# Kernel tuning notes

Measured on AMD Instinct MI355X. Metric: run time of the kernel, lower is better.

## Reference

```python
import jax, jax.numpy as jnp
import numpy as np

B, T, CIN, H = 128, 512, 512, 256  # batch, time, conv-in channels, hidden
G = 4 * H  # LSTM gate width (i,f,g,o in PyTorch order)


def setup_inputs() -> dict:
    key = jax.random.key(0)
    ks = jax.random.split(key, 13)
    s = 0.05
    return {
        "x": jax.random.normal(ks[0], (B, CIN, T, 1), jnp.float32),
        "w1": jax.random.normal(ks[1], (H, CIN), jnp.float32) * s,  # 1x1 conv -> [out,in]
        "b1": jax.random.normal(ks[2], (H,), jnp.float32) * s,
        "w2": jax.random.normal(ks[3], (H, H), jnp.float32) * s,
        "b2": jax.random.normal(ks[4], (H,), jnp.float32) * s,
        "w_ih_f": jax.random.normal(ks[5], (G, H), jnp.float32) * s,
        "w_hh_f": jax.random.normal(ks[6], (G, H), jnp.float32) * s,
        "b_ih_f": jax.random.normal(ks[7], (G,), jnp.float32) * s,
        "b_hh_f": jax.random.normal(ks[8], (G,), jnp.float32) * s,
        "w_ih_b": jax.random.normal(ks[9], (G, H), jnp.float32) * s,
        "w_hh_b": jax.random.normal(ks[10], (G, H), jnp.float32) * s,
        "b_ih_b": jax.random.normal(ks[11], (G,), jnp.float32) * s,
        "b_hh_b": jax.random.normal(ks[12], (G,), jnp.float32) * s,
    }


def _lstm(xg, w_hh):
    """Run LSTM over time. xg: [B,T,4H] = x@w_ih.T + b_ih + b_hh (precomputed)."""
    h0 = jnp.zeros((xg.shape[0], w_hh.shape[1]), xg.dtype)

    def step(carry, g_in):
        h, c = carry
        g = g_in + h @ w_hh.T
        i, f, gg, o = jnp.split(g, 4, axis=-1)
        c = jax.nn.sigmoid(f) * c + jax.nn.sigmoid(i) * jnp.tanh(gg)
        h = jax.nn.sigmoid(o) * jnp.tanh(c)
        return (h, c), h

    _, hs = jax.lax.scan(step, (h0, h0), jnp.swapaxes(xg, 0, 1))  # [T,B,H]
    return jnp.swapaxes(hs, 0, 1)  # [B,T,H]


def reference(x, w1, b1, w2, b2, w_ih_f, w_hh_f, b_ih_f, b_hh_f,
              w_ih_b, w_hh_b, b_ih_b, b_hh_b):
    # 1x1 convs == per-pixel GEMMs
    y = jax.nn.relu(jnp.einsum('bchw,oc->bohw', x, w1) + b1[None, :, None, None])
    y = jax.nn.relu(jnp.einsum('bchw,oc->bohw', y, w2) + b2[None, :, None, None])
    # torch .view(B, H_dim, -1) on contiguous [B,256,T,1] -> [B,T,256] (row-major reinterpret)
    seq = y.reshape(y.shape[0], y.shape[2], -1)  # [B,T,256]
    # forward direction
    xg_f = jnp.einsum('btd,gd->btg', seq, w_ih_f) + b_ih_f + b_hh_f
    h_f = _lstm(xg_f, w_hh_f)
    # backward direction: reverse time, run, reverse back
    seq_r = seq[:, ::-1, :]
    xg_b = jnp.einsum('btd,gd->btg', seq_r, w_ih_b) + b_ih_b + b_hh_b
    h_b = _lstm(xg_b, w_hh_b)[:, ::-1, :]
    out = jnp.concatenate([h_f, h_b], axis=-1)  # [B,T,2H]
    # dropout is identity at inference; return last timestep
    return out[:, -1, :]
```

## Files before the change

### kernel.cpp

```cpp
#include <hip/hip_runtime.h>
#include <math.h>

#define BATCH 128
#define TT 512
#define CIN 512
#define HID 256
#define GG 1024

typedef _Float16 half2_t __attribute__((ext_vector_type(2)));
typedef _Float16 half8_t __attribute__((ext_vector_type(8)));
typedef float f32x4_t __attribute__((ext_vector_type(4)));

__device__ __forceinline__ float sigf(float x) { return 1.f / (1.f + __expf(-x)); }
__device__ __forceinline__ float tanhf_(float x) {
    float a = fabsf(x);
    float e = __expf(-2.f * a);
    float r = (1.f - e) / (1.f + e);
    return copysignf(r, x);
}
__device__ __forceinline__ float fdot2_(half2_t a, half2_t b, float c) {
#if __has_builtin(__builtin_amdgcn_fdot2)
    return __builtin_amdgcn_fdot2(a, b, c, false);
#else
    return c + (float)a.x * (float)b.x + (float)a.y * (float)b.y;
#endif
}

__global__ void prep_cast(const float* __restrict__ w1, const float* __restrict__ w2,
                          const float* __restrict__ wih, const float* __restrict__ bih,
                          const float* __restrict__ bhh,
                          _Float16* __restrict__ w1h, _Float16* __restrict__ w2h,
                          _Float16* __restrict__ wihh, float* __restrict__ bsum)
{
    const int i = blockIdx.x * 256 + threadIdx.x;
    if (i < 131072) w1h[i] = (_Float16)w1[i];
    if (i < 65536)  w2h[i] = (_Float16)w2[i];
    if (i < 262144) wihh[i] = (_Float16)wih[i];
    if (i < 1024)   bsum[i] = bih[i] + bhh[i];
}

__global__ __launch_bounds__(256) void cast_transpose_x(
    const float* __restrict__ x, _Float16* __restrict__ xt)
{
    const int b = blockIdx.z, c0 = blockIdx.y * 64, t0 = blockIdx.x * 64;
    __shared__ float tl[64][68];
    const float* xb = x + (size_t)b * CIN * TT;
    const int tid = threadIdx.x;
    const int lt = (tid & 15) * 4, lc = tid >> 4;
    #pragma unroll
    for (int r = 0; r < 4; ++r) {
        const int c = lc + r * 16;
        float4 v = *(const float4*)(xb + (size_t)(c0 + c) * TT + t0 + lt);
        tl[c][lt] = v.x; tl[c][lt + 1] = v.y; tl[c][lt + 2] = v.z; tl[c][lt + 3] = v.w;
    }
    __syncthreads();
    const int trow = tid >> 2, coff = (tid & 3) * 16;
    _Float16 o[16];
    #pragma unroll
    for (int i = 0; i < 16; ++i) o[i] = (_Float16)tl[coff + i][trow];
    _Float16* dst = xt + (size_t)b * TT * CIN + (size_t)(t0 + trow) * CIN + c0 + coff;
    *(float4*)dst = *(float4*)&o[0];
    *(float4*)(dst + 8) = *(float4*)&o[8];
}

template <int RELU, int BIASROW>
__global__ __launch_bounds__(256, 4) void mfma_nt(
    const _Float16* __restrict__ A, const _Float16* __restrict__ B,
    const float* __restrict__ bias, _Float16* __restrict__ C,
    int M, int N, int K, long sA, long sB, long sC)
{
    __shared__ __align__(16) char smem[34816];
    _Float16 (*As)[40] = (_Float16(*)[40])smem;
    _Float16 (*Bs)[40] = (_Float16(*)[40])(smem + 10240);
    float (*Ct)[132] = (float(*)[132])smem;

    const int nb = blockIdx.z;
    A += (size_t)nb * sA; B += (size_t)nb * sB; C += (size_t)nb * sC;
    const int m0 = blockIdx.y * 128, n0 = blockIdx.x * 128;
    const int tid = threadIdx.x;
    const int wave = tid >> 6, lane = tid & 63;
    const int quad = lane >> 4, l15 = lane & 15;
    const int wm = (wave >> 1) * 64, wn = (wave & 1) * 64;
    const int srow = tid >> 1, sko = (tid & 1) * 16;

    f32x4_t acc[4][4];
    const f32x4_t zz = {0.f, 0.f, 0.f, 0.f};
    #pragma unroll
    for (int i = 0; i < 4; ++i)
        #pragma unroll
        for (int j = 0; j < 4; ++j) acc[i][j] = zz;

    for (int k0 = 0; k0 < K; k0 += 32) {
        {
            const float4* ga = (const float4*)(A + (size_t)(m0 + srow) * K + k0 + sko);
            float4 a0 = ga[0], a1 = ga[1];
            const float4* gb = (const float4*)(B + (size_t)(n0 + srow) * K + k0 + sko);
            float4 b0 = gb[0], b1 = gb[1];
            *(float4*)&As[srow][sko] = a0; *(float4*)&As[srow][sko + 8] = a1;
            *(float4*)&Bs[srow][sko] = b0; *(float4*)&Bs[srow][sko + 8] = b1;
        }
        __syncthreads();
        half8_t af[4], bf[4];
        #pragma unroll
        for (int i = 0; i < 4; ++i) af[i] = *(const half8_t*)&As[wm + i * 16 + l15][quad * 8];
        #pragma unroll
        for (int j = 0; j < 4; ++j) bf[j] = *(const half8_t*)&Bs[wn + j * 16 + l15][quad * 8];
        #pragma unroll
        for (int i = 0; i < 4; ++i)
            #pragma unroll
            for (int j = 0; j < 4; ++j)
                acc[i][j] = __builtin_amdgcn_mfma_f32_16x16x32_f16(af[i], bf[j], acc[i][j], 0, 0, 0);
        __syncthreads();
    }

    const int trow = tid >> 2, coff = (tid & 3) * 32;
    float bcol[32];
    if (!BIASROW) {
        #pragma unroll
        for (int i = 0; i < 8; ++i)
            *(float4*)&bcol[i * 4] = *(const float4*)&bias[n0 + coff + i * 4];
    }
    #pragma unroll
    for (int p = 0; p < 2; ++p) {
        if (p) __syncthreads();
        if ((wave >> 1) == p) {
            #pragma unroll
            for (int mi = 0; mi < 4; ++mi)
                #pragma unroll
                for (int ni = 0; ni < 4; ++ni)
                    #pragma unroll
                    for (int r = 0; r < 4; ++r)
                        Ct[mi * 16 + quad * 4 + r][wn + ni * 16 + l15] = acc[mi][ni][r];
        }
        __syncthreads();
        float brow = 0.f;
        if (BIASROW) brow = bias[m0 + p * 64 + trow];
        float vv[32];
        #pragma unroll
        for (int i = 0; i < 8; ++i) *(float4*)&vv[i * 4] = *(float4*)&Ct[trow][coff + i * 4];
        _Float16 o[32];
        #pragma unroll
        for (int i = 0; i < 32; ++i) {
            float v = vv[i] + (BIASROW ? brow : bcol[i]);
            if (RELU) v = fmaxf(v, 0.f);
            o[i] = (_Float16)v;
        }
        _Float16* dst = C + (size_t)(m0 + p * 64 + trow) * N + n0 + coff;
        #pragma unroll
        for (int i = 0; i < 4; ++i) *(float4*)(dst + i * 8) = *(float4*)&o[i * 8];
    }
}

__global__ __launch_bounds__(1024, 4) void lstm_scan5(
    const _Float16* __restrict__ xg, const float* __restrict__ whh,
    float* __restrict__ out, unsigned long long* __restrict__ xb)
{
    const int tid = threadIdx.x;
    const int bid = blockIdx.x;
    const int is_hi = (bid >= 128) ? 1 : 0;
    const int g = is_hi ? bid - 128 : bid;
    const int q4 = tid >> 8;
    const int s = tid & 255;
    const int u = s & 127;
    const int rowA = (s >> 7) * 256 + is_hi * 128 + u;
    const int rowB = rowA + 512;

    __shared__ __align__(16) unsigned int hsh[128];
    __shared__ float psh[2048];

    half2_t wA[32], wB[32];
    {
        const float4* pa = (const float4*)(whh + (size_t)rowA * 256 + q4 * 64);
        const float4* pb = (const float4*)(whh + (size_t)rowB * 256 + q4 * 64);
        #pragma unroll
        for (int k = 0; k < 16; ++k) {
            float4 a = pa[k], b = pb[k];
            wA[2 * k + 0] = half2_t{(_Float16)a.x, (_Float16)a.y};
            wA[2 * k + 1] = half2_t{(_Float16)a.z, (_Float16)a.w};
            wB[2 * k + 0] = half2_t{(_Float16)b.x, (_Float16)b.y};
            wB[2 * k + 1] = half2_t{(_Float16)b.z, (_Float16)b.w};
        }
    }
    if (tid < 128) hsh[tid] = 0u;
    const _Float16* xgb = xg + (size_t)g * TT * GG;
    float xA = 0.f, xB = 0.f;
    if (q4 == 0) { xA = (float)xgb[rowA]; xB = (float)xgb[rowB]; }
    float c0 = 0.f, c1 = 0.f, hk0 = 0.f, hk1 = 0.f;
    __syncthreads();

    for (int t = 0; t < TT; ++t) {
        const float vA = xA, vB = xB;
        if (q4 == 0 && t < TT - 1) {
            xA = (float)xgb[(size_t)(t + 1) * GG + rowA];
            xB = (float)xgb[(size_t)(t + 1) * GG + rowB];
        }
        float aA0 = 0.f, aA1 = 0.f, aB0 = 0.f, aB1 = 0.f;
        const float4* hp = (const float4*)hsh + q4 * 8;
        #pragma unroll
        for (int kk = 0; kk < 8; ++kk) {
            const float4 hv = hp[kk];
            const half2_t h0 = __builtin_bit_cast(half2_t, hv.x);
            const half2_t h1 = __builtin_bit_cast(half2_t, hv.y);
            const half2_t h2 = __builtin_bit_cast(half2_t, hv.z);
            const half2_t h3 = __builtin_bit_cast(half2_t, hv.w);
            aA0 = fdot2_(wA[4 * kk + 0], h0, aA0);
            aA1 = fdot2_(wA[4 * kk + 1], h1, aA1);
            aA0 = fdot2_(wA[4 * kk + 2], h2, aA0);
            aA1 = fdot2_(wA[4 * kk + 3], h3, aA1);
            aB0 = fdot2_(wB[4 * kk + 0], h0, aB0);
            aB1 = fdot2_(wB[4 * kk + 1], h1, aB1);
            aB0 = fdot2_(wB[4 * kk + 2], h2, aB0);
            aB1 = fdot2_(wB[4 * kk + 3], h3, aB1);
        }
        psh[q4 * 512 + s]       = aA0 + aA1 + vA;
        psh[q4 * 512 + 256 + s] = aB0 + aB1 + vB;
        __syncthreads();
        if (tid < 64) {
            const int l = tid;
            float2 gate[4];
            #pragma unroll
            for (int gg = 0; gg < 4; ++gg) {
                float2 sum = {0.f, 0.f};
                #pragma unroll
                for (int qq = 0; qq < 4; ++qq) {
                    const float2 v = *(const float2*)&psh[qq * 512 + gg * 128 + 2 * l];
                    sum.x += v.x; sum.y += v.y;
                }
                gate[gg] = sum;
            }
            const float i0 = sigf(gate[0].x), i1 = sigf(gate[0].y);
            const float f0 = sigf(gate[1].x), f1 = sigf(gate[1].y);
            const float g0 = tanhf_(gate[2].x), g1 = tanhf_(gate[2].y);
            const float o0 = sigf(gate[3].x), o1 = sigf(gate[3].y);
            c0 = f0 * c0 + i0 * g0;  hk0 = o0 * tanhf_(c0);
            c1 = f1 * c1 + i1 * g1;  hk1 = o1 * tanhf_(c1);
            const unsigned int u0 =
                (unsigned int)__builtin_bit_cast(unsigned short, (_Float16)hk0);
            const unsigned int u1 =
                (unsigned int)__builtin_bit_cast(unsigned short, (_Float16)hk1);
            hsh[is_hi * 64 + l] = u0 | (u1 << 16);
            if (t < TT - 1) {
                const unsigned int tg = (unsigned int)(t + 1) << 16;
                const unsigned long long pk =
                    ((unsigned long long)(tg | u1) << 32) | (unsigned long long)(tg | u0);
                __hip_atomic_store(&xb[((size_t)g * 2 + is_hi) * 64 + l], pk,
                                   __ATOMIC_RELAXED, __HIP_MEMORY_SCOPE_AGENT);
                asm volatile("" ::: "memory");
                unsigned long long v;
                const unsigned long long* src = &xb[((size_t)g * 2 + (1 - is_hi)) * 64 + l];
                for (;;) {
                    v = __hip_atomic_load(src, __ATOMIC_RELAXED,
                                          __HIP_MEMORY_SCOPE_AGENT);
                    if ((((v >> 16) & 0xFFFFu) == (unsigned)(t + 1)) &&
                        ((unsigned)(v >> 48) == (unsigned)(t + 1))) break;
                    __builtin_amdgcn_s_sleep(1);
                }
                hsh[(1 - is_hi) * 64 + l] =
                    (unsigned int)(v & 0xFFFFu) |
                    ((unsigned int)((v >> 32) & 0xFFFFu) << 16);
            }
        }
        __syncthreads();
    }
    if (tid < 64) {
        out[(size_t)g * 512 + is_hi * 128 + 2 * tid + 0] = hk0;
        out[(size_t)g * 512 + is_hi * 128 + 2 * tid + 1] = hk1;
    }
}

__global__ __launch_bounds__(256) void lstm_back_last(
    const _Float16* __restrict__ y2h, const float* __restrict__ wih,
    const float* __restrict__ bih, const float* __restrict__ bhh,
    float* __restrict__ out)
{
    const int b = blockIdx.x;
    const int t = threadIdx.x;
    __shared__ float s[256];
    s[t] = (float)y2h[(size_t)b * (HID * TT) + (TT - 1) * HID + t];
    __syncthreads();
    float acc[4];
    #pragma unroll
    for (int q = 0; q < 4; ++q) acc[q] = bih[t + q * 256] + bhh[t + q * 256];
    #pragma unroll
    for (int q = 0; q < 4; ++q) {
        const float* w = wih + (size_t)(t + q * 256) * 256;
        float a = acc[q];
        for (int k = 0; k < 256; k += 4) {
            const float4 w4 = *(const float4*)&w[k];
            const float4 h4 = *(const float4*)&s[k];
            a += w4.x * h4.x; a += w4.y * h4.y;
            a += w4.z * h4.z; a += w4.w * h4.w;
        }
        acc[q] = a;
    }
    const float i = sigf(acc[0]);
    const float g = tanhf_(acc[2]), o = sigf(acc[3]);
    const float c = i * g;
    const float h = o * tanhf_(c);
    out[(size_t)b * 512 + 256 + t] = h;
}

extern "C" void kernel_launch(void* const* d_in, const int* in_sizes, int n_in,
                              void* d_out, int out_size, void* d_ws, size_t ws_size,
                              hipStream_t stream) {
    const float* x      = (const float*)d_in[0];
    const float* w1     = (const float*)d_in[1];
    const float* b1     = (const float*)d_in[2];
    const float* w2     = (const float*)d_in[3];
    const float* b2     = (const float*)d_in[4];
    const float* w_ih_f = (const float*)d_in[5];
    const float* w_hh_f = (const float*)d_in[6];
    const float* b_ih_f = (const float*)d_in[7];
    const float* b_hh_f = (const float*)d_in[8];
    const float* w_ih_b = (const float*)d_in[9];
    const float* b_ih_b = (const float*)d_in[11];
    const float* b_hh_b = (const float*)d_in[12];
    float* out = (float*)d_out;

    char* ws = (char*)d_ws;
    _Float16* xgh  = (_Float16*)(ws);
    _Float16* xt   = (_Float16*)(ws + 134217728);
    _Float16* y1t  = (_Float16*)(ws + 201326592);
    _Float16* y2h  = (_Float16*)(ws + 234881024);
    _Float16* w1h  = (_Float16*)(ws + 268435456);
    _Float16* w2h  = (_Float16*)(ws + 268697600);
    _Float16* wihh = (_Float16*)(ws + 268828672);
    float*    bsum = (float*)   (ws + 269352960);
    unsigned long long* xb = (unsigned long long*)(ws + 269357056);

    prep_cast<<<1024, 256, 0, stream>>>(w1, w2, w_ih_f, b_ih_f, b_hh_f,
                                        w1h, w2h, wihh, bsum);
    cast_transpose_x<<<dim3(8, 8, BATCH), 256, 0, stream>>>(x, xt);
    mfma_nt<1, 0><<<dim3(2, 4, BATCH), 256, 0, stream>>>(
        xt, w1h, b1, y1t, 512, 256, 512, 512L * 512, 0, 512L * 256);
    mfma_nt<1, 1><<<dim3(4, 2, BATCH), 256, 0, stream>>>(
        w2h, y1t, b2, y2h, 256, 512, 256, 0, 512L * 256, 256L * 512);
    mfma_nt<0, 0><<<dim3(8, 512, 1), 256, 0, stream>>>(
        y2h, wihh, bsum, xgh, 65536, 1024, 256, 0, 0, 0);
    lstm_back_last<<<BATCH, 256, 0, stream>>>(y2h, w_ih_b, b_ih_b, b_hh_b, out);
    lstm_scan5<<<256, 1024, 0, stream>>>(xgh, w_hh_f, out, xb);
}
```

Before: 1.282 ms.

## Interleave two batch rows per LSTM block to overlap dot products with cross-block handoff

Each scan block now handles two batch rows, processed in an interleaved schedule. While one wave does the activation and publishes h for batch A, the other waves compute the recurrent dot products for batch B, and a dedicated wave polls the partner block's h. This hides the inter-block exchange latency and the serial activation phase behind useful work. The cost is half as many blocks, more syncthreads per step and double the shared buffers.

```diff
diff --git a/kernel.cpp b/kernel.cpp
--- a/kernel.cpp
+++ b/kernel.cpp
@@ -151,22 +151,24 @@
     }
 }
 
-__global__ __launch_bounds__(1024, 4) void lstm_scan5(
+__global__ __launch_bounds__(1024, 4) void lstm_scan6(
     const _Float16* __restrict__ xg, const float* __restrict__ whh,
     float* __restrict__ out, unsigned long long* __restrict__ xb)
 {
     const int tid = threadIdx.x;
     const int bid = blockIdx.x;
-    const int is_hi = (bid >= 128) ? 1 : 0;
-    const int g = is_hi ? bid - 128 : bid;
+    const int is_hi = (bid >= 64) ? 1 : 0;
+    const int p = is_hi ? bid - 64 : bid;
+    const int gb0 = 2 * p, gb1 = 2 * p + 1;
     const int q4 = tid >> 8;
     const int s = tid & 255;
     const int u = s & 127;
     const int rowA = (s >> 7) * 256 + is_hi * 128 + u;
     const int rowB = rowA + 512;
-
-    __shared__ __align__(16) unsigned int hsh[128];
-    __shared__ float psh[2048];
+    const int wv = tid >> 6, l = tid & 63;
+
+    __shared__ __align__(16) unsigned int hsh[2][128];
+    __shared__ __align__(16) float psh[2][2048];
 
     half2_t wA[32], wB[32];
     {
@@ -181,21 +183,21 @@
             wB[2 * k + 1] = half2_t{(_Float16)b.z, (_Float16)b.w};
         }
     }
-    if (tid < 128) hsh[tid] = 0u;
-    const _Float16* xgb = xg + (size_t)g * TT * GG;
-    float xA = 0.f, xB = 0.f;
-    if (q4 == 0) { xA = (float)xgb[rowA]; xB = (float)xgb[rowB]; }
+    if (tid < 256) hsh[tid >> 7][tid & 127] = 0u;
+
+    const _Float16* xgb0 = xg + (size_t)gb0 * TT * GG;
+    const _Float16* xgb1 = xg + (size_t)gb1 * TT * GG;
+    float x0A = 0.f, x0B = 0.f, x1A = 0.f, x1B = 0.f;
+    if (q4 == 1) {
+        x0A = (float)xgb0[rowA]; x0B = (float)xgb0[rowB];
+        x1A = (float)xgb1[rowA]; x1B = (float)xgb1[rowB];
+    }
     float c0 = 0.f, c1 = 0.f, hk0 = 0.f, hk1 = 0.f;
     __syncthreads();
 
-    for (int t = 0; t < TT; ++t) {
-        const float vA = xA, vB = xB;
-        if (q4 == 0 && t < TT - 1) {
-            xA = (float)xgb[(size_t)(t + 1) * GG + rowA];
-            xB = (float)xgb[(size_t)(t + 1) * GG + rowB];
-        }
+    auto dot_phase = [&](int bb, float vA, float vB) {
         float aA0 = 0.f, aA1 = 0.f, aB0 = 0.f, aB1 = 0.f;
-        const float4* hp = (const float4*)hsh + q4 * 8;
+        const float4* hp = (const float4*)&hsh[bb][0] + q4 * 8;
         #pragma unroll
         for (int kk = 0; kk < 8; ++kk) {
             const float4 hv = hp[kk];
@@ -212,59 +214,82 @@
             aB0 = fdot2_(wB[4 * kk + 2], h2, aB0);
             aB1 = fdot2_(wB[4 * kk + 3], h3, aB1);
         }
-        psh[q4 * 512 + s]       = aA0 + aA1 + vA;
-        psh[q4 * 512 + 256 + s] = aB0 + aB1 + vB;
-        __syncthreads();
-        if (tid < 64) {
-            const int l = tid;
-            float2 gate[4];
+        psh[bb][q4 * 512 + s]       = aA0 + aA1 + vA;
+        psh[bb][q4 * 512 + 256 + s] = aB0 + aB1 + vB;
+    };
+
+    auto act_publish = [&](int bb, int gbb, int t) {
+        float2 gate[4];
+        #pragma unroll
+        for (int gg = 0; gg < 4; ++gg) {
+            float2 sum = {0.f, 0.f};
             #pragma unroll
-            for (int gg = 0; gg < 4; ++gg) {
-                float2 sum = {0.f, 0.f};
-                #pragma unroll
-                for (int qq = 0; qq < 4; ++qq) {
-                    const float2 v = *(const float2*)&psh[qq * 512 + gg * 128 + 2 * l];
-                    sum.x += v.x; sum.y += v.y;
-                }
-                gate[gg] = sum;
+            for (int qq = 0; qq < 4; ++qq) {
+                const float2 v = *(const float2*)&psh[bb][qq * 512 + gg * 128 + 2 * l];
+                sum.x += v.x; sum.y += v.y;
             }
-            const float i0 = sigf(gate[0].x), i1 = sigf(gate[0].y);
-            const float f0 = sigf(gate[1].x), f1 = sigf(gate[1].y);
-            const float g0 = tanhf_(gate[2].x), g1 = tanhf_(gate[2].y);
-            const float o0 = sigf(gate[3].x), o1 = sigf(gate[3].y);
-            c0 = f0 * c0 + i0 * g0;  hk0 = o0 * tanhf_(c0);
-            c1 = f1 * c1 + i1 * g1;  hk1 = o1 * tanhf_(c1);
-            const unsigned int u0 =
-                (unsigned int)__builtin_bit_cast(unsigned short, (_Float16)hk0);
-            const unsigned int u1 =
-                (unsigned int)__builtin_bit_cast(unsigned short, (_Float16)hk1);
-            hsh[is_hi * 64 + l] = u0 | (u1 << 16);
-            if (t < TT - 1) {
-                const unsigned int tg = (unsigned int)(t + 1) << 16;
-                const unsigned long long pk =
-                    ((unsigned long long)(tg | u1) << 32) | (unsigned long long)(tg | u0);
-                __hip_atomic_store(&xb[((size_t)g * 2 + is_hi) * 64 + l], pk,
-                                   __ATOMIC_RELAXED, __HIP_MEMORY_SCOPE_AGENT);
-                asm volatile("" ::: "memory");
-                unsigned long long v;
-                const unsigned long long* src = &xb[((size_t)g * 2 + (1 - is_hi)) * 64 + l];
-                for (;;) {
-                    v = __hip_atomic_load(src, __ATOMIC_RELAXED,
-                                          __HIP_MEMORY_SCOPE_AGENT);
-                    if ((((v >> 16) & 0xFFFFu) == (unsigned)(t + 1)) &&
-                        ((unsigned)(v >> 48) == (unsigned)(t + 1))) break;
-                    __builtin_amdgcn_s_sleep(1);
-                }
-                hsh[(1 - is_hi) * 64 + l] =
-                    (unsigned int)(v & 0xFFFFu) |
-                    ((unsigned int)((v >> 32) & 0xFFFFu) << 16);
-            }
-        }
-        __syncthreads();
-    }
-    if (tid < 64) {
-        out[(size_t)g * 512 + is_hi * 128 + 2 * tid + 0] = hk0;
-        out[(size_t)g * 512 + is_hi * 128 + 2 * tid + 1] = hk1;
+            gate[gg] = sum;
+        }
+        const float i0 = sigf(gate[0].x), i1 = sigf(gate[0].y);
+        const float f0 = sigf(gate[1].x), f1 = sigf(gate[1].y);
+        const float q0 = tanhf_(gate[2].x), q1 = tanhf_(gate[2].y);
+        const float o0 = sigf(gate[3].x), o1 = sigf(gate[3].y);
+        c0 = f0 * c0 + i0 * q0;  hk0 = o0 * tanhf_(c0);
+        c1 = f1 * c1 + i1 * q1;  hk1 = o1 * tanhf_(c1);
+        const unsigned int u0 =
+            (unsigned int)__builtin_bit_cast(unsigned short, (_Float16)hk0);
+        const unsigned int u1 =
+            (unsigned int)__builtin_bit_cast(unsigned short, (_Float16)hk1);
+        if (t < TT - 1) {
+            const unsigned int tg = (unsigned int)(t + 1) << 16;
+            const unsigned long long pk =
+                ((unsigned long long)(tg | u1) << 32) | (unsigned long long)(tg | u0);
+            __hip_atomic_store(&xb[((size_t)gbb * 2 + is_hi) * 64 + l], pk,
+                               __ATOMIC_RELAXED, __HIP_MEMORY_SCOPE_AGENT);
+            asm volatile("" ::: "memory");
+        }
+        hsh[bb][is_hi * 64 + l] = u0 | (u1 << 16);
+    };
+
+    auto poll_partner = [&](int bb, int gbb, unsigned int tag) {
+        const unsigned long long* src = &xb[((size_t)gbb * 2 + (1 - is_hi)) * 64 + l];
+        unsigned long long v;
+        for (;;) {
+            v = __hip_atomic_load(src, __ATOMIC_RELAXED, __HIP_MEMORY_SCOPE_AGENT);
+            if ((((v >> 16) & 0xFFFFu) == tag) && ((unsigned)(v >> 48) == tag)) break;
+            __builtin_amdgcn_s_sleep(1);
+        }
+        hsh[bb][(1 - is_hi) * 64 + l] =
+            (unsigned int)(v & 0xFFFFu) | ((unsigned int)((v >> 32) & 0xFFFFu) << 16);
+    };
+
+    for (int t = 0; t < TT; ++t) {
+        const float v0A = x0A, v0B = x0B, v1A = x1A, v1B = x1B;
+        if (q4 == 1 && t < TT - 1) {
+            x0A = (float)xgb0[(size_t)(t + 1) * GG + rowA];
+            x0B = (float)xgb0[(size_t)(t + 1) * GG + rowB];
+            x1A = (float)xgb1[(size_t)(t + 1) * GG + rowA];
+            x1B = (float)xgb1[(size_t)(t + 1) * GG + rowB];
+        }
+        if (wv == 15 && t > 0) poll_partner(1, gb1, (unsigned int)t);
+        dot_phase(0, v0A, v0B);
+        __syncthreads();
+
+        if (wv == 0) act_publish(0, gb0, t);
+        dot_phase(1, v1A, v1B);
+        __syncthreads();
+
+        if (wv == 1) act_publish(1, gb1, t);
+        if (wv == 15 && t < TT - 1) poll_partner(0, gb0, (unsigned int)(t + 1));
+        __syncthreads();
+    }
+    if (wv == 0) {
+        out[(size_t)gb0 * 512 + is_hi * 128 + 2 * l + 0] = hk0;
+        out[(size_t)gb0 * 512 + is_hi * 128 + 2 * l + 1] = hk1;
+    }
+    if (wv == 1) {
+        out[(size_t)gb1 * 512 + is_hi * 128 + 2 * l + 0] = hk0;
+        out[(size_t)gb1 * 512 + is_hi * 128 + 2 * l + 1] = hk1;
     }
 }
 
@@ -338,5 +363,5 @@
     mfma_nt<0, 0><<<dim3(8, 512, 1), 256, 0, stream>>>(
         y2h, wihh, bsum, xgh, 65536, 1024, 256, 0, 0, 0);
     lstm_back_last<<<BATCH, 256, 0, stream>>>(y2h, w_ih_b, b_ih_b, b_hh_b, out);
-    lstm_scan5<<<256, 1024, 0, stream>>>(xgh, w_hh_f, out, xb);
-}
+    lstm_scan6<<<128, 1024, 0, stream>>>(xgh, w_hh_f, out, xb);
+}
```

After: 1.630 ms. +27.2%, slower.

## Run each batch's LSTM scan in one workgroup, dropping cross-block handshakes

Applied to the files above, without the earlier changes.

Replaces the two-workgroups-per-batch-row LSTM scan, which swapped hidden-state halves through global atomics and spin-waits every step, with one 1024-thread workgroup per batch row. Each thread now computes all four gates for one hidden unit. Three gate weight slices sit in registers and the output-gate weights go in a swizzled 128KB LDS buffer. The gate pre-activations are staged in a double-buffered LDS slot. This removes per-step inter-block sync latency, but halves the number of workgroups (128 instead of 256) and adds more per-thread work plus LDS weight reads each step.

```diff
diff --git a/kernel.cpp b/kernel.cpp
--- a/kernel.cpp
+++ b/kernel.cpp
@@ -151,51 +151,73 @@
     }
 }
 
-__global__ __launch_bounds__(1024, 4) void lstm_scan5(
+__global__ __launch_bounds__(1024, 4) void lstm_scan7(
     const _Float16* __restrict__ xg, const float* __restrict__ whh,
-    float* __restrict__ out, unsigned long long* __restrict__ xb)
-{
+    float* __restrict__ out)
+{
+    __shared__ __align__(16) _Float16 wlds[256 * 256];
+    __shared__ __align__(16) float psh[4096];
+    __shared__ __align__(16) _Float16 xgsh[2][1024];
+    __shared__ __align__(16) _Float16 hshh[256];
+
     const int tid = threadIdx.x;
-    const int bid = blockIdx.x;
-    const int is_hi = (bid >= 128) ? 1 : 0;
-    const int g = is_hi ? bid - 128 : bid;
-    const int q4 = tid >> 8;
-    const int s = tid & 255;
-    const int u = s & 127;
-    const int rowA = (s >> 7) * 256 + is_hi * 128 + u;
-    const int rowB = rowA + 512;
-
-    __shared__ __align__(16) unsigned int hsh[128];
-    __shared__ float psh[2048];
-
-    half2_t wA[32], wB[32];
+    const int b   = blockIdx.x;
+    const int q4  = tid >> 8;
+    const int s   = tid & 255;
+    const _Float16* xgb = xg + (size_t)b * TT * GG;
+
     {
-        const float4* pa = (const float4*)(whh + (size_t)rowA * 256 + q4 * 64);
-        const float4* pb = (const float4*)(whh + (size_t)rowB * 256 + q4 * 64);
+        const int sr = tid >> 2, c4 = tid & 3;
+        const float* wr = whh + (size_t)(768 + sr) * 256;
+        #pragma unroll
+        for (int j = 0; j < 8; ++j) {
+            const int g = c4 * 8 + j;
+            const float4 w0 = *(const float4*)&wr[g * 8 + 0];
+            const float4 w1 = *(const float4*)&wr[g * 8 + 4];
+            float4 pk;
+            half2_t* pp = (half2_t*)&pk;
+            pp[0] = half2_t{(_Float16)w0.x, (_Float16)w0.y};
+            pp[1] = half2_t{(_Float16)w0.z, (_Float16)w0.w};
+            pp[2] = half2_t{(_Float16)w1.x, (_Float16)w1.y};
+            pp[3] = half2_t{(_Float16)w1.z, (_Float16)w1.w};
+            *(float4*)((char*)wlds + sr * 512 + ((g ^ (sr & 7)) << 4)) = pk;
+        }
+    }
+    half2_t wI[32], wF[32], wGt[32];
+    {
+        const float4* pi = (const float4*)(whh + (size_t)(s)*256 + q4 * 64);
+        const float4* pf = (const float4*)(whh + (size_t)(s + 256) * 256 + q4 * 64);
+        const float4* pg = (const float4*)(whh + (size_t)(s + 512) * 256 + q4 * 64);
         #pragma unroll
         for (int k = 0; k < 16; ++k) {
-            float4 a = pa[k], b = pb[k];
-            wA[2 * k + 0] = half2_t{(_Float16)a.x, (_Float16)a.y};
-            wA[2 * k + 1] = half2_t{(_Float16)a.z, (_Float16)a.w};
-            wB[2 * k + 0] = half2_t{(_Float16)b.x, (_Float16)b.y};
-            wB[2 * k + 1] = half2_t{(_Float16)b.z, (_Float16)b.w};
-        }
-    }
-    if (tid < 128) hsh[tid] = 0u;
-    const _Float16* xgb = xg + (size_t)g * TT * GG;
-    float xA = 0.f, xB = 0.f;
-    if (q4 == 0) { xA = (float)xgb[rowA]; xB = (float)xgb[rowB]; }
-    float c0 = 0.f, c1 = 0.f, hk0 = 0.f, hk1 = 0.f;
+            const float4 a = pi[k];
+            wI[2 * k + 0] = half2_t{(_Float16)a.x, (_Float16)a.y};
+            wI[2 * k + 1] = half2_t{(_Float16)a.z, (_Float16)a.w};
+            const float4 f = pf[k];
+            wF[2 * k + 0] = half2_t{(_Float16)f.x, (_Float16)f.y};
+            wF[2 * k + 1] = half2_t{(_Float16)f.z, (_Float16)f.w};
+            const float4 g = pg[k];
+            wGt[2 * k + 0] = half2_t{(_Float16)g.x, (_Float16)g.y};
+            wGt[2 * k + 1] = half2_t{(_Float16)g.z, (_Float16)g.w};
+        }
+    }
+    if (tid < 128) ((unsigned int*)hshh)[tid] = 0u;
+    if (q4 == 3) {
+        *(uint2*)&xgsh[0][4 * s] = *(const uint2*)&xgb[4 * s];
+    }
+    float c = 0.f, hlast = 0.f;
     __syncthreads();
 
+    const float4* hp = (const float4*)hshh + q4 * 8;
+    const char* wob = (const char*)wlds + s * 512 + q4 * 128;
+    const int sw3 = s & 7;
+
     for (int t = 0; t < TT; ++t) {
-        const float vA = xA, vB = xB;
-        if (q4 == 0 && t < TT - 1) {
-            xA = (float)xgb[(size_t)(t + 1) * GG + rowA];
-            xB = (float)xgb[(size_t)(t + 1) * GG + rowB];
-        }
-        float aA0 = 0.f, aA1 = 0.f, aB0 = 0.f, aB1 = 0.f;
-        const float4* hp = (const float4*)hsh + q4 * 8;
+        if (q4 == 3 && t + 1 < TT) {
+            *(uint2*)&xgsh[(t + 1) & 1][4 * s] =
+                *(const uint2*)&xgb[(size_t)(t + 1) * GG + 4 * s];
+        }
+        float aI = 0.f, aF = 0.f, aG = 0.f, aO = 0.f;
         #pragma unroll
         for (int kk = 0; kk < 8; ++kk) {
             const float4 hv = hp[kk];
@@ -203,69 +225,51 @@
             const half2_t h1 = __builtin_bit_cast(half2_t, hv.y);
             const half2_t h2 = __builtin_bit_cast(half2_t, hv.z);
             const half2_t h3 = __builtin_bit_cast(half2_t, hv.w);
-            aA0 = fdot2_(wA[4 * kk + 0], h0, aA0);
-            aA1 = fdot2_(wA[4 * kk + 1], h1, aA1);
-            aA0 = fdot2_(wA[4 * kk + 2], h2, aA0);
-            aA1 = fdot2_(wA[4 * kk + 3], h3, aA1);
-            aB0 = fdot2_(wB[4 * kk + 0], h0, aB0);
-            aB1 = fdot2_(wB[4 * kk + 1], h1, aB1);
-            aB0 = fdot2_(wB[4 * kk + 2], h2, aB0);
-            aB1 = fdot2_(wB[4 * kk + 3], h3, aB1);
-        }
-        psh[q4 * 512 + s]       = aA0 + aA1 + vA;
-        psh[q4 * 512 + 256 + s] = aB0 + aB1 + vB;
-        __syncthreads();
-        if (tid < 64) {
-            const int l = tid;
-            float2 gate[4];
-            #pragma unroll
-            for (int gg = 0; gg < 4; ++gg) {
-                float2 sum = {0.f, 0.f};
-                #pragma unroll
-                for (int qq = 0; qq < 4; ++qq) {
-                    const float2 v = *(const float2*)&psh[qq * 512 + gg * 128 + 2 * l];
-                    sum.x += v.x; sum.y += v.y;
-                }
-                gate[gg] = sum;
-            }
-            const float i0 = sigf(gate[0].x), i1 = sigf(gate[0].y);
-            const float f0 = sigf(gate[1].x), f1 = sigf(gate[1].y);
-            const float g0 = tanhf_(gate[2].x), g1 = tanhf_(gate[2].y);
-            const float o0 = sigf(gate[3].x), o1 = sigf(gate[3].y);
-            c0 = f0 * c0 + i0 * g0;  hk0 = o0 * tanhf_(c0);
-            c1 = f1 * c1 + i1 * g1;  hk1 = o1 * tanhf_(c1);
-            const unsigned int u0 =
-                (unsigned int)__builtin_bit_cast(unsigned short, (_Float16)hk0);
-            const unsigned int u1 =
-                (unsigned int)__builtin_bit_cast(unsigned short, (_Float16)hk1);
-            hsh[is_hi * 64 + l] = u0 | (u1 << 16);
-            if (t < TT - 1) {
-                const unsigned int tg = (unsigned int)(t + 1) << 16;
-                const unsigned long long pk =
-                    ((unsigned long long)(tg | u1) << 32) | (unsigned long long)(tg | u0);
-                __hip_atomic_store(&xb[((size_t)g * 2 + is_hi) * 64 + l], pk,
-                                   __ATOMIC_RELAXED, __HIP_MEMORY_SCOPE_AGENT);
-                asm volatile("" ::: "memory");
-                unsigned long long v;
-                const unsigned long long* src = &xb[((size_t)g * 2 + (1 - is_hi)) * 64 + l];
-                for (;;) {
-                    v = __hip_atomic_load(src, __ATOMIC_RELAXED,
-                                          __HIP_MEMORY_SCOPE_AGENT);
-                    if ((((v >> 16) & 0xFFFFu) == (unsigned)(t + 1)) &&
-                        ((unsigned)(v >> 48) == (unsigned)(t + 1))) break;
-                    __builtin_amdgcn_s_sleep(1);
-                }
-                hsh[(1 - is_hi) * 64 + l] =
-                    (unsigned int)(v & 0xFFFFu) |
-                    ((unsigned int)((v >> 32) & 0xFFFFu) << 16);
-            }
-        }
-        __syncthreads();
-    }
-    if (tid < 64) {
-        out[(size_t)g * 512 + is_hi * 128 + 2 * tid + 0] = hk0;
-        out[(size_t)g * 512 + is_hi * 128 + 2 * tid + 1] = hk1;
-    }
+            const float4 wv = *(const float4*)(wob + ((kk ^ sw3) << 4));
+            const half2_t o0 = __builtin_bit_cast(half2_t, wv.x);
+            const half2_t o1 = __builtin_bit_cast(half2_t, wv.y);
+            const half2_t o2 = __builtin_bit_cast(half2_t, wv.z);
+            const half2_t o3 = __builtin_bit_cast(half2_t, wv.w);
+            aI = fdot2_(wI[4 * kk + 0], h0, aI);
+            aI = fdot2_(wI[4 * kk + 1], h1, aI);
+            aI = fdot2_(wI[4 * kk + 2], h2, aI);
+            aI = fdot2_(wI[4 * kk + 3], h3, aI);
+            aF = fdot2_(wF[4 * kk + 0], h0, aF);
+            aF = fdot2_(wF[4 * kk + 1], h1, aF);
+            aF = fdot2_(wF[4 * kk + 2], h2, aF);
+            aF = fdot2_(wF[4 * kk + 3], h3, aF);
+            aG = fdot2_(wGt[4 * kk + 0], h0, aG);
+            aG = fdot2_(wGt[4 * kk + 1], h1, aG);
+            aG = fdot2_(wGt[4 * kk + 2], h2, aG);
+            aG = fdot2_(wGt[4 * kk + 3], h3, aG);
+            aO = fdot2_(o0, h0, aO);
+            aO = fdot2_(o1, h1, aO);
+            aO = fdot2_(o2, h2, aO);
+            aO = fdot2_(o3, h3, aO);
+        }
+        psh[q4 * 1024 + s]       = aI;
+        psh[q4 * 1024 + s + 256] = aF;
+        psh[q4 * 1024 + s + 512] = aG;
+        psh[q4 * 1024 + s + 768] = aO;
+        __syncthreads();
+        if (tid < 256) {
+            const int cur = t & 1;
+            const float gi = psh[s] + psh[1024 + s] + psh[2048 + s] + psh[3072 + s]
+                             + (float)xgsh[cur][s];
+            const float gf = psh[s + 256] + psh[1280 + s] + psh[2304 + s] + psh[3328 + s]
+                             + (float)xgsh[cur][s + 256];
+            const float gq = psh[s + 512] + psh[1536 + s] + psh[2560 + s] + psh[3584 + s]
+                             + (float)xgsh[cur][s + 512];
+            const float go = psh[s + 768] + psh[1792 + s] + psh[2816 + s] + psh[3840 + s]
+                             + (float)xgsh[cur][s + 768];
+            const float iv = sigf(gi), fv = sigf(gf), gv = tanhf_(gq), ov = sigf(go);
+            c = fv * c + iv * gv;
+            hlast = ov * tanhf_(c);
+            hshh[s] = (_Float16)hlast;
+        }
+        __syncthreads();
+    }
+    if (tid < 256) out[(size_t)b * 512 + s] = hlast;
 }
 
 __global__ __launch_bounds__(256) void lstm_back_last(
@@ -326,7 +330,6 @@
     _Float16* w2h  = (_Float16*)(ws + 268697600);
     _Float16* wihh = (_Float16*)(ws + 268828672);
     float*    bsum = (float*)   (ws + 269352960);
-    unsigned long long* xb = (unsigned long long*)(ws + 269357056);
 
     prep_cast<<<1024, 256, 0, stream>>>(w1, w2, w_ih_f, b_ih_f, b_hh_f,
                                         w1h, w2h, wihh, bsum);
@@ -338,5 +341,5 @@
     mfma_nt<0, 0><<<dim3(8, 512, 1), 256, 0, stream>>>(
         y2h, wihh, bsum, xgh, 65536, 1024, 256, 0, 0, 0);
     lstm_back_last<<<BATCH, 256, 0, stream>>>(y2h, w_ih_b, b_ih_b, b_hh_b, out);
-    lstm_scan5<<<256, 1024, 0, stream>>>(xgh, w_hh_f, out, xb);
-}
+    lstm_scan7<<<BATCH, 1024, 0, stream>>>(xgh, w_hh_f, out);
+}
```

Result: slower. 1.422 ms (+11.0%).

## Pipeline cross-block spin-wait loads and double-buffer mailbox by step parity

Applied to the files above, without the earlier changes.

Reworks the inter-block hidden-state exchange in the LSTM scan. The mailbox is now double-buffered by timestep parity and zeroed in lstm_back_last. It reuses the y1t workspace region, which is dead by the time the scan runs. The poll is an inline-assembly loop that keeps three pairs of global loads in flight instead of a serialized load-sleep loop, with a fallback to the old atomic poll after a bounded number of tries. The aim is lower per-step handshake latency on the serial critical path. The cost is fragile hand-written asm, and the parity buffers rely on the peer never running more than one step ahead.

```diff
diff --git a/kernel.cpp b/kernel.cpp
--- a/kernel.cpp
+++ b/kernel.cpp
@@ -151,9 +151,9 @@
     }
 }
 
-__global__ __launch_bounds__(1024, 4) void lstm_scan5(
+__global__ __launch_bounds__(1024, 4) void lstm_scan11(
     const _Float16* __restrict__ xg, const float* __restrict__ whh,
-    float* __restrict__ out, unsigned long long* __restrict__ xb)
+    float* __restrict__ out, unsigned long long* __restrict__ mb)
 {
     const int tid = threadIdx.x;
     const int bid = blockIdx.x;
@@ -238,26 +238,105 @@
                 (unsigned int)__builtin_bit_cast(unsigned short, (_Float16)hk0);
             const unsigned int u1 =
                 (unsigned int)__builtin_bit_cast(unsigned short, (_Float16)hk1);
-            hsh[is_hi * 64 + l] = u0 | (u1 << 16);
             if (t < TT - 1) {
-                const unsigned int tg = (unsigned int)(t + 1) << 16;
+                const unsigned int want = (unsigned int)(t + 1);
+                const unsigned int tg = want << 16;
                 const unsigned long long pk =
                     ((unsigned long long)(tg | u1) << 32) | (unsigned long long)(tg | u0);
-                __hip_atomic_store(&xb[((size_t)g * 2 + is_hi) * 64 + l], pk,
+                const size_t par = (size_t)(want & 1u) * 16384;
+                __hip_atomic_store(&mb[par + ((size_t)g * 2 + is_hi) * 64 + l], pk,
                                    __ATOMIC_RELAXED, __HIP_MEMORY_SCOPE_AGENT);
                 asm volatile("" ::: "memory");
-                unsigned long long v;
-                const unsigned long long* src = &xb[((size_t)g * 2 + (1 - is_hi)) * 64 + l];
-                for (;;) {
-                    v = __hip_atomic_load(src, __ATOMIC_RELAXED,
-                                          __HIP_MEMORY_SCOPE_AGENT);
-                    if ((((v >> 16) & 0xFFFFu) == (unsigned)(t + 1)) &&
-                        ((unsigned)(v >> 48) == (unsigned)(t + 1))) break;
-                    __builtin_amdgcn_s_sleep(1);
+                hsh[is_hi * 64 + l] = u0 | (u1 << 16);
+                const unsigned long long srcaddr = (unsigned long long)
+                    &mb[par + ((size_t)g * 2 + (1 - is_hi)) * 64 + l];
+                unsigned int r0, r1, hit;
+                {
+                    unsigned int pa0, pa1, pb0, pb1, pc0, pc1, t0, t1, cnt;
+                    asm volatile(
+                        "global_load_dword %[a0], %[ad], off sc1\n\t"
+                        "global_load_dword %[a1], %[ad], off offset:4 sc1\n\t"
+                        "global_load_dword %[b0], %[ad], off sc1\n\t"
+                        "global_load_dword %[b1], %[ad], off offset:4 sc1\n\t"
+                        "global_load_dword %[c0], %[ad], off sc1\n\t"
+                        "global_load_dword %[c1], %[ad], off offset:4 sc1\n\t"
+                        "s_mov_b32 %[cnt], 0\n"
+                        "PL%=:\n\t"
+                        "s_waitcnt vmcnt(4)\n\t"
+                        "v_lshrrev_b32 %[t0], 16, %[a0]\n\t"
+                        "v_lshrrev_b32 %[t1], 16, %[a1]\n\t"
+                        "v_cmp_ne_u32 vcc, %[t0], %[wt]\n\t"
+                        "s_cbranch_vccnz MA%=\n\t"
+                        "v_cmp_ne_u32 vcc, %[t1], %[wt]\n\t"
+                        "s_cbranch_vccnz MA%=\n\t"
+                        "v_mov_b32 %[r0], %[a0]\n\t"
+                        "v_mov_b32 %[r1], %[a1]\n\t"
+                        "s_mov_b32 %[hit], 1\n\t"
+                        "s_branch PD%=\n"
+                        "MA%=:\n\t"
+                        "global_load_dword %[a0], %[ad], off sc1\n\t"
+                        "global_load_dword %[a1], %[ad], off offset:4 sc1\n\t"
+                        "s_waitcnt vmcnt(4)\n\t"
+                        "v_lshrrev_b32 %[t0], 16, %[b0]\n\t"
+                        "v_lshrrev_b32 %[t1], 16, %[b1]\n\t"
+                        "v_cmp_ne_u32 vcc, %[t0], %[wt]\n\t"
+                        "s_cbranch_vccnz MB%=\n\t"
+                        "v_cmp_ne_u32 vcc, %[t1], %[wt]\n\t"
+                        "s_cbranch_vccnz MB%=\n\t"
+                        "v_mov_b32 %[r0], %[b0]\n\t"
+                        "v_mov_b32 %[r1], %[b1]\n\t"
+                        "s_mov_b32 %[hit], 1\n\t"
+                        "s_branch PD%=\n"
+                        "MB%=:\n\t"
+                        "global_load_dword %[b0], %[ad], off sc1\n\t"
+                        "global_load_dword %[b1], %[ad], off offset:4 sc1\n\t"
+                        "s_waitcnt vmcnt(4)\n\t"
+                        "v_lshrrev_b32 %[t0], 16, %[c0]\n\t"
+                        "v_lshrrev_b32 %[t1], 16, %[c1]\n\t"
+                        "v_cmp_ne_u32 vcc, %[t0], %[wt]\n\t"
+                        "s_cbranch_vccnz MC%=\n\t"
+                        "v_cmp_ne_u32 vcc, %[t1], %[wt]\n\t"
+                        "s_cbranch_vccnz MC%=\n\t"
+                        "v_mov_b32 %[r0], %[c0]\n\t"
+                        "v_mov_b32 %[r1], %[c1]\n\t"
+                        "s_mov_b32 %[hit], 1\n\t"
+                        "s_branch PD%=\n"
+                        "MC%=:\n\t"
+                        "global_load_dword %[c0], %[ad], off sc1\n\t"
+                        "global_load_dword %[c1], %[ad], off offset:4 sc1\n\t"
+                        "s_add_u32 %[cnt], %[cnt], 1\n\t"
+                        "s_cmp_lt_u32 %[cnt], 24\n\t"
+                        "s_cbranch_scc1 PL%=\n\t"
+                        "s_mov_b32 %[hit], 0\n"
+                        "PD%=:\n\t"
+                        "s_waitcnt vmcnt(0)"
+                        : [a0]"=&v"(pa0), [a1]"=&v"(pa1), [b0]"=&v"(pb0),
+                          [b1]"=&v"(pb1), [c0]"=&v"(pc0), [c1]"=&v"(pc1),
+                          [t0]"=&v"(t0), [t1]"=&v"(t1),
+                          [r0]"=&v"(r0), [r1]"=&v"(r1),
+                          [hit]"=&s"(hit), [cnt]"=&s"(cnt)
+                        : [ad]"v"(srcaddr), [wt]"v"(want)
+                        : "vcc", "memory");
+                }
+                if (!hit) {
+                    const unsigned long long* src =
+                        (const unsigned long long*)srcaddr;
+                    for (;;) {
+                        unsigned long long v = __hip_atomic_load(
+                            src, __ATOMIC_RELAXED, __HIP_MEMORY_SCOPE_AGENT);
+                        if ((((v >> 16) & 0xFFFFu) == want) &&
+                            ((unsigned)(v >> 48) == want)) {
+                            r0 = (unsigned int)v;
+                            r1 = (unsigned int)(v >> 32);
+                            break;
+                        }
+                        __builtin_amdgcn_s_sleep(1);
+                    }
                 }
                 hsh[(1 - is_hi) * 64 + l] =
-                    (unsigned int)(v & 0xFFFFu) |
-                    ((unsigned int)((v >> 32) & 0xFFFFu) << 16);
+                    (r0 & 0xFFFFu) | ((r1 & 0xFFFFu) << 16);
+            } else {
+                hsh[is_hi * 64 + l] = u0 | (u1 << 16);
             }
         }
         __syncthreads();
@@ -271,10 +350,11 @@
 __global__ __launch_bounds__(256) void lstm_back_last(
     const _Float16* __restrict__ y2h, const float* __restrict__ wih,
     const float* __restrict__ bih, const float* __restrict__ bhh,
-    float* __restrict__ out)
+    float* __restrict__ out, unsigned long long* __restrict__ mb)
 {
     const int b = blockIdx.x;
     const int t = threadIdx.x;
+    mb[b * 256 + t] = 0ull;
     __shared__ float s[256];
     s[t] = (float)y2h[(size_t)b * (HID * TT) + (TT - 1) * HID + t];
     __syncthreads();
@@ -326,7 +406,7 @@
     _Float16* w2h  = (_Float16*)(ws + 268697600);
     _Float16* wihh = (_Float16*)(ws + 268828672);
     float*    bsum = (float*)   (ws + 269352960);
-    unsigned long long* xb = (unsigned long long*)(ws + 269357056);
+    unsigned long long* mb = (unsigned long long*)(ws + 201326592);
 
     prep_cast<<<1024, 256, 0, stream>>>(w1, w2, w_ih_f, b_ih_f, b_hh_f,
                                         w1h, w2h, wihh, bsum);
@@ -337,6 +417,6 @@
         w2h, y1t, b2, y2h, 256, 512, 256, 0, 512L * 256, 256L * 512);
     mfma_nt<0, 0><<<dim3(8, 512, 1), 256, 0, stream>>>(
         y2h, wihh, bsum, xgh, 65536, 1024, 256, 0, 0, 0);
-    lstm_back_last<<<BATCH, 256, 0, stream>>>(y2h, w_ih_b, b_ih_b, b_hh_b, out);
-    lstm_scan5<<<256, 1024, 0, stream>>>(xgh, w_hh_f, out, xb);
-}
+    lstm_back_last<<<BATCH, 256, 0, stream>>>(y2h, w_ih_b, b_ih_b, b_hh_b, out, mb);
+    lstm_scan11<<<256, 1024, 0, stream>>>(xgh, w_hh_f, out, mb);
+}
```

New measurement: 1.305 ms. No clear change (+1.8%).
